# Kernel optimization log

Measured on AMD Instinct MI355X. Metric: run time of the kernel, lower is better.

Reference implementation:

```python
import jax, jax.numpy as jnp
import numpy as np

# ranges from init_kwargs
T2P_RANGE = (1.0, 500.0)
B1_RANGE = (0.2, 1.6)

NX, NY = 256, 256
NUM_T2S, NUM_B1S, ETL = 100, 30, 16


def _nan_to_num0(x):
    # torch.nan_to_num(x, nan=0.0, posinf=0.0); inputs here are non-negative so
    # neginf never occurs, but we zero it too for safety.
    return jnp.nan_to_num(x, nan=0.0, posinf=0.0, neginf=0.0)


def setup_inputs() -> dict:
    key = jax.random.key(0)
    k1, k2, k3 = jax.random.split(key, 3)
    slice_signal = jax.random.uniform(k1, (NX, NY, ETL), dtype=jnp.float32)
    db_mag = jax.random.uniform(k2, (NUM_T2S, NUM_B1S, ETL), dtype=jnp.float32)
    db_t2s_ms = jnp.linspace(1.0, 1000.0, NUM_T2S, dtype=jnp.float32)
    db_b1s = jnp.linspace(0.2, 1.6, NUM_B1S, dtype=jnp.float32)
    delta_t_t2p_ms = 9.0 * jnp.arange(1, ETL + 1, dtype=jnp.float32)  # echo times
    estimates = jax.random.uniform(k3, (2, NX, NY), dtype=jnp.float32)
    return {
        "slice_signal": slice_signal,
        "db_mag": db_mag,
        "db_t2s_ms": db_t2s_ms,
        "db_b1s": db_b1s,
        "delta_t_t2p_ms": delta_t_t2p_ms,
        "estimates": estimates,
    }


def reference(slice_signal, db_mag, db_t2s_ms, db_b1s, delta_t_t2p_ms, estimates):
    etl = slice_signal.shape[-1]
    sig = _nan_to_num0(slice_signal / jnp.linalg.norm(slice_signal, axis=-1, keepdims=True))
    sig = sig.reshape(-1, etl)  # (P, etl)

    # b1 map from estimates[1], scaled to b1_range
    b1 = B1_RANGE[0] + (B1_RANGE[1] - B1_RANGE[0]) * estimates[1]  # (nx, ny)
    # TV term: torch.gradient default == numpy.gradient (central diff interior,
    # one-sided edges)
    g0, g1 = jnp.gradient(b1)
    f_2 = jnp.sum(jnp.abs(g0) + jnp.abs(g1))

    # nearest-neighbor B1 dictionary lookup (non-differentiable gather)
    b1_flat = b1.reshape(-1)  # (P,)
    b1_idx = jnp.argmin((b1_flat[:, None] - db_b1s[None, :]) ** 2, axis=-1)  # (P,)
    db = db_mag[:, b1_idx]  # (T2, P, etl)

    # eta = exp(-dt / t2p), t2p from estimates[0] scaled to t2p_range
    t2p = T2P_RANGE[0] + (T2P_RANGE[1] - T2P_RANGE[0]) * estimates[0].reshape(-1)  # (P,)
    eta = jnp.exp(-delta_t_t2p_ms[None, :] / t2p[:, None])  # (P, etl)

    s_db = db * eta[None]  # (T2, P, etl)
    s_db = _nan_to_num0(s_db / jnp.linalg.norm(s_db, axis=-1, keepdims=True))

    l2_min = jnp.linalg.norm(s_db - sig[None], axis=-1)  # (T2, P)
    f_1 = jnp.sum(jnp.linalg.norm(l2_min, axis=-1))  # sum over T2 of per-T2 norms over pixels
    return f_1 + f_2
```

## Files before the change

### kernel.cpp

```cpp
#include <hip/hip_runtime.h>
#include <math.h>

constexpr int NXc = 256, NYc = 256, ETLc = 16, NTc = 100, NBc = 30;
constexpr int NPIX = NXc * NYc;
constexpr int TMAX = 13;
constexpr int RSTRIDE = 20;
constexpr int PST = 532;
constexpr int QST = 132;


__global__ __launch_bounds__(1024, 8) void k_main(
    const float* __restrict__ sig,
    const float* __restrict__ db_mag,
    const float* __restrict__ dtt,
    const float* __restrict__ est,
    float* __restrict__ ws_f1,
    float* __restrict__ ws_f2)
{
    const int tid      = threadIdx.x;
    const int pixgroup = blockIdx.x & 63;
    const int tc       = blockIdx.x >> 6;
    const int p = (pixgroup << 10) | tid;
    const int x = p >> 8;
    const int y = p & 255;
    const int t0   = (tc < 4) ? tc * 13 : 52 + (tc - 4) * 12;
    const int tcnt = (tc < 4) ? 13 : 12;
    const int lane = tid & 63;

    alignas(16) __shared__ float lds[TMAX * NBc * RSTRIDE];
    __shared__ float s_p[TMAX * PST];
    __shared__ float s_f2[16];

    {
        const float4* gsrc = reinterpret_cast<const float4*>(db_mag + (size_t)t0 * (NBc * ETLc));
        for (int i = tid; i < tcnt * 120; i += 1024) {
            const int ttl = i / 120;
            const int rem = i - ttl * 120;
            *reinterpret_cast<float4*>(
                &lds[ttl * (NBc * RSTRIDE) + (rem >> 2) * RSTRIDE + (rem & 3) * 4]) = gsrc[i];
        }
    }

    const float4* sp = reinterpret_cast<const float4*>(sig + (size_t)p * ETLc);
    float s[16];
    {
        float4 a = sp[0], b = sp[1], c = sp[2], d = sp[3];
        s[0]=a.x; s[1]=a.y; s[2]=a.z;  s[3]=a.w;
        s[4]=b.x; s[5]=b.y; s[6]=b.z;  s[7]=b.w;
        s[8]=c.x; s[9]=c.y; s[10]=c.z; s[11]=c.w;
        s[12]=d.x; s[13]=d.y; s[14]=d.z; s[15]=d.w;
    }
    float snrm2 = 0.f;
#pragma unroll
    for (int e = 0; e < 16; ++e) snrm2 = fmaf(s[e], s[e], snrm2);
    const float sig2  = (snrm2 > 0.f) ? 1.0f : 0.0f;
    const float srinv = (snrm2 > 0.f) ? __builtin_amdgcn_rsqf(snrm2) : 0.0f;
    float sgn[16];
#pragma unroll
    for (int e = 0; e < 16; ++e) sgn[e] = s[e] * srinv;

    const float est0 = est[p];
    const float t2p  = 1.0f + 499.0f * est0;
    const float nrcp = -__builtin_amdgcn_rcpf(t2p);
    float eta[16];
#pragma unroll
    for (int e = 0; e < 16; ++e) eta[e] = __expf(dtt[e] * nrcp);

    const float est1 = est[NPIX + p];
    float kf = roundf(est1 * 29.0f);
    kf = fminf(fmaxf(kf, 0.0f), 29.0f);
    const int jb = (int)kf;

    if (tc == 0) {
        const float* e1 = est + NPIX;
        const float c = 0.2f + 1.4f * est1;
        float g0, g1;
        if (x == 0)            g0 = (0.2f + 1.4f * e1[p + 256]) - c;
        else if (x == NXc - 1) g0 = c - (0.2f + 1.4f * e1[p - 256]);
        else                   g0 = 0.5f * ((0.2f + 1.4f * e1[p + 256]) - (0.2f + 1.4f * e1[p - 256]));
        if (y == 0)            g1 = (0.2f + 1.4f * e1[p + 1]) - c;
        else if (y == NYc - 1) g1 = c - (0.2f + 1.4f * e1[p - 1]);
        else                   g1 = 0.5f * ((0.2f + 1.4f * e1[p + 1]) - (0.2f + 1.4f * e1[p - 1]));
        float r = fabsf(g0) + fabsf(g1);
#pragma unroll
        for (int m = 32; m; m >>= 1) r += __shfl_xor(r, m, 64);
        if (lane == 0) s_f2[tid >> 6] = r;
    }

    __syncthreads();
    if (tc == 0 && tid < 4)
        ws_f2[(pixgroup << 2) + tid] =
            (s_f2[tid*4+0] + s_f2[tid*4+1]) + (s_f2[tid*4+2] + s_f2[tid*4+3]);

#pragma unroll 1
    for (int tt = 0; tt < tcnt; ++tt) {
        const float4* lp = reinterpret_cast<const float4*>(
            &lds[tt * (NBc * RSTRIDE) + jb * RSTRIDE]);
        float4 a = lp[0], b = lp[1], c = lp[2], d = lp[3];
        float dbr[16];
        dbr[0]=a.x; dbr[1]=a.y; dbr[2]=a.z;  dbr[3]=a.w;
        dbr[4]=b.x; dbr[5]=b.y; dbr[6]=b.z;  dbr[7]=b.w;
        dbr[8]=c.x; dbr[9]=c.y; dbr[10]=c.z; dbr[11]=c.w;
        dbr[12]=d.x; dbr[13]=d.y; dbr[14]=d.z; dbr[15]=d.w;

        float nrm2 = 0.f, dotv = 0.f;
#pragma unroll
        for (int e = 0; e < 16; ++e) {
            float v = dbr[e] * eta[e];
            nrm2 = fmaf(v, v, nrm2);
            dotv = fmaf(v, sgn[e], dotv);
        }
        float l2sq;
        if (nrm2 > 0.f) l2sq = sig2 + 1.0f - 2.0f * dotv * __builtin_amdgcn_rsqf(nrm2);
        else            l2sq = sig2;
        float r = (l2sq < 0.f) ? 0.f : l2sq;

        r += __shfl_xor(r, 1, 64);
        if ((lane & 1) == 0)
            s_p[tt * PST + (tid >> 8) * QST + ((tid >> 1) & 127)] = r;
    }
    __syncthreads();

    if (tid < tcnt * 64) {
        const int t = tid >> 6;
        const int q = (tid >> 4) & 3;
        const int j = tid & 15;
        const float* row = &s_p[t * PST + q * QST + j];
        float b = 0.f;
#pragma unroll
        for (int k = 0; k < 8; ++k) b += row[k * 16];
        b += __shfl_xor(b, 1, 64);
        b += __shfl_xor(b, 2, 64);
        b += __shfl_xor(b, 4, 64);
        b += __shfl_xor(b, 8, 64);
        if (j == 0) ws_f1[(size_t)(t0 + t) * 256 + (pixgroup << 2) + q] = b;
    }
}

__global__ __launch_bounds__(512) void k_final(
    const float* __restrict__ ws_f1,
    const float* __restrict__ ws_f2,
    float* __restrict__ out)
{
    const int tid = threadIdx.x;
    const int t = tid >> 2, g = tid & 3;
    float sum = 0.f;
    if (t < NTc) {
        const float4* p4 = reinterpret_cast<const float4*>(ws_f1 + (size_t)t * 256 + g * 64);
#pragma unroll
        for (int i = 0; i < 16; ++i) { float4 v = p4[i]; sum += (v.x + v.y) + (v.z + v.w); }
    }
    sum += __shfl_xor(sum, 1, 64);
    sum += __shfl_xor(sum, 2, 64);

    __shared__ float s_sq[128];
    if (tid < 128) s_sq[tid] = 0.f;
    __syncthreads();
    if (g == 0 && t < NTc) s_sq[t] = sqrtf(sum);
    __syncthreads();

    if (tid < 64) {
        float v = s_sq[tid] + s_sq[tid + 64];
        v += (ws_f2[tid] + ws_f2[tid + 64]) + (ws_f2[tid + 128] + ws_f2[tid + 192]);
#pragma unroll
        for (int m = 32; m; m >>= 1) v += __shfl_xor(v, m, 64);
        if (tid == 0) out[0] = v;
    }
}

extern "C" void kernel_launch(void* const* d_in, const int* in_sizes, int n_in,
                              void* d_out, int out_size, void* d_ws, size_t ws_size,
                              hipStream_t stream) {
    const float* sig    = (const float*)d_in[0];
    const float* db_mag = (const float*)d_in[1];
    const float* dtt    = (const float*)d_in[4];
    const float* est    = (const float*)d_in[5];
    float* out = (float*)d_out;

    float* ws_f1 = (float*)d_ws;
    float* ws_f2 = ws_f1 + (size_t)NTc * 256;

    k_main <<<dim3(64 * 8), dim3(1024), 0, stream>>>(sig, db_mag, dtt, est, ws_f1, ws_f2);
    k_final<<<dim3(1),      dim3(512),  0, stream>>>(ws_f1, ws_f2, out);
}
```

Measured before the change: 23.39 us.

## Sort pixels by B1 bin per block and read dictionary rows from global

Each block now counting-sorts its 1024 pixels by B1 bin, using LDS atomics for a histogram and rank assignment. Threads are then remapped so that neighbouring lanes share the same dictionary row. The LDS staging of the db_mag slab is removed, and each iteration reads its 16-float row straight from global memory. The aim is to avoid the LDS fill and the scattered LDS reads, relying on cache broadcast for the now-uniform rows. In exchange it adds extra barriers, atomics and permuted, less coalesced loads of the signal and estimates.

After: 28.26 us. +20.8%, slower.

```diff
diff --git a/kernel.cpp b/kernel.cpp
--- a/kernel.cpp
+++ b/kernel.cpp
@@ -4,7 +4,6 @@
 constexpr int NXc = 256, NYc = 256, ETLc = 16, NTc = 100, NBc = 30;
 constexpr int NPIX = NXc * NYc;
 constexpr int TMAX = 13;
-constexpr int RSTRIDE = 20;
 constexpr int PST = 532;
 constexpr int QST = 132;
 
@@ -27,53 +26,25 @@
     const int tcnt = (tc < 4) ? 13 : 12;
     const int lane = tid & 63;
 
-    alignas(16) __shared__ float lds[TMAX * NBc * RSTRIDE];
     __shared__ float s_p[TMAX * PST];
     __shared__ float s_f2[16];
-
-    {
-        const float4* gsrc = reinterpret_cast<const float4*>(db_mag + (size_t)t0 * (NBc * ETLc));
-        for (int i = tid; i < tcnt * 120; i += 1024) {
-            const int ttl = i / 120;
-            const int rem = i - ttl * 120;
-            *reinterpret_cast<float4*>(
-                &lds[ttl * (NBc * RSTRIDE) + (rem >> 2) * RSTRIDE + (rem & 3) * 4]) = gsrc[i];
-        }
-    }
-
-    const float4* sp = reinterpret_cast<const float4*>(sig + (size_t)p * ETLc);
-    float s[16];
-    {
-        float4 a = sp[0], b = sp[1], c = sp[2], d = sp[3];
-        s[0]=a.x; s[1]=a.y; s[2]=a.z;  s[3]=a.w;
-        s[4]=b.x; s[5]=b.y; s[6]=b.z;  s[7]=b.w;
-        s[8]=c.x; s[9]=c.y; s[10]=c.z; s[11]=c.w;
-        s[12]=d.x; s[13]=d.y; s[14]=d.z; s[15]=d.w;
-    }
-    float snrm2 = 0.f;
-#pragma unroll
-    for (int e = 0; e < 16; ++e) snrm2 = fmaf(s[e], s[e], snrm2);
-    const float sig2  = (snrm2 > 0.f) ? 1.0f : 0.0f;
-    const float srinv = (snrm2 > 0.f) ? __builtin_amdgcn_rsqf(snrm2) : 0.0f;
-    float sgn[16];
-#pragma unroll
-    for (int e = 0; e < 16; ++e) sgn[e] = s[e] * srinv;
-
-    const float est0 = est[p];
-    const float t2p  = 1.0f + 499.0f * est0;
-    const float nrcp = -__builtin_amdgcn_rcpf(t2p);
-    float eta[16];
-#pragma unroll
-    for (int e = 0; e < 16; ++e) eta[e] = __expf(dtt[e] * nrcp);
-
-    const float est1 = est[NPIX + p];
-    float kf = roundf(est1 * 29.0f);
-    kf = fminf(fmaxf(kf, 0.0f), 29.0f);
-    const int jb = (int)kf;
+    __shared__ int s_hist[NBc];
+    __shared__ int s_base[NBc];
+    __shared__ unsigned short s_ord[1024];
+
+    if (tid < NBc) s_hist[tid] = 0;
+
+    const float est1_own = est[NPIX + p];
+    float kfo = roundf(est1_own * 29.0f);
+    kfo = fminf(fmaxf(kfo, 0.0f), 29.0f);
+    const int jb_own = (int)kfo;
+
+    __syncthreads();
+    atomicAdd(&s_hist[jb_own], 1);
 
     if (tc == 0) {
         const float* e1 = est + NPIX;
-        const float c = 0.2f + 1.4f * est1;
+        const float c = 0.2f + 1.4f * est1_own;
         float g0, g1;
         if (x == 0)            g0 = (0.2f + 1.4f * e1[p + 256]) - c;
         else if (x == NXc - 1) g0 = c - (0.2f + 1.4f * e1[p - 256]);
@@ -88,15 +59,59 @@
     }
 
     __syncthreads();
+    if (tid == 0) {
+        int a = 0;
+#pragma unroll
+        for (int j = 0; j < NBc; ++j) { s_base[j] = a; a += s_hist[j]; }
+    }
     if (tc == 0 && tid < 4)
         ws_f2[(pixgroup << 2) + tid] =
             (s_f2[tid*4+0] + s_f2[tid*4+1]) + (s_f2[tid*4+2] + s_f2[tid*4+3]);
-
+    __syncthreads();
+    {
+        const int rank = atomicAdd(&s_base[jb_own], 1);
+        s_ord[rank] = (unsigned short)tid;
+    }
+    __syncthreads();
+
+    const int q = (pixgroup << 10) | (int)s_ord[tid];
+
+    const float4* sp = reinterpret_cast<const float4*>(sig + (size_t)q * ETLc);
+    float s[16];
+    {
+        float4 a = sp[0], b = sp[1], c = sp[2], d = sp[3];
+        s[0]=a.x; s[1]=a.y; s[2]=a.z;  s[3]=a.w;
+        s[4]=b.x; s[5]=b.y; s[6]=b.z;  s[7]=b.w;
+        s[8]=c.x; s[9]=c.y; s[10]=c.z; s[11]=c.w;
+        s[12]=d.x; s[13]=d.y; s[14]=d.z; s[15]=d.w;
+    }
+    float snrm2 = 0.f;
+#pragma unroll
+    for (int e = 0; e < 16; ++e) snrm2 = fmaf(s[e], s[e], snrm2);
+    const float sig2  = (snrm2 > 0.f) ? 1.0f : 0.0f;
+    const float srinv = (snrm2 > 0.f) ? __builtin_amdgcn_rsqf(snrm2) : 0.0f;
+    float sgn[16];
+#pragma unroll
+    for (int e = 0; e < 16; ++e) sgn[e] = s[e] * srinv;
+
+    const float est0 = est[q];
+    const float t2p  = 1.0f + 499.0f * est0;
+    const float nrcp = -__builtin_amdgcn_rcpf(t2p);
+    float eta[16];
+#pragma unroll
+    for (int e = 0; e < 16; ++e) eta[e] = __expf(dtt[e] * nrcp);
+
+    const float est1 = est[NPIX + q];
+    float kf = roundf(est1 * 29.0f);
+    kf = fminf(fmaxf(kf, 0.0f), 29.0f);
+    const int jb = (int)kf;
+
+    const float* dbj = db_mag + (size_t)jb * ETLc;
 #pragma unroll 1
     for (int tt = 0; tt < tcnt; ++tt) {
-        const float4* lp = reinterpret_cast<const float4*>(
-            &lds[tt * (NBc * RSTRIDE) + jb * RSTRIDE]);
-        float4 a = lp[0], b = lp[1], c = lp[2], d = lp[3];
+        const float4* dp = reinterpret_cast<const float4*>(
+            dbj + (size_t)(t0 + tt) * (NBc * ETLc));
+        float4 a = dp[0], b = dp[1], c = dp[2], d = dp[3];
         float dbr[16];
         dbr[0]=a.x; dbr[1]=a.y; dbr[2]=a.z;  dbr[3]=a.w;
         dbr[4]=b.x; dbr[5]=b.y; dbr[6]=b.z;  dbr[7]=b.w;
@@ -123,9 +138,9 @@
 
     if (tid < tcnt * 64) {
         const int t = tid >> 6;
-        const int q = (tid >> 4) & 3;
+        const int q4 = (tid >> 4) & 3;
         const int j = tid & 15;
-        const float* row = &s_p[t * PST + q * QST + j];
+        const float* row = &s_p[t * PST + q4 * QST + j];
         float b = 0.f;
 #pragma unroll
         for (int k = 0; k < 8; ++k) b += row[k * 16];
@@ -133,7 +148,7 @@
         b += __shfl_xor(b, 2, 64);
         b += __shfl_xor(b, 4, 64);
         b += __shfl_xor(b, 8, 64);
-        if (j == 0) ws_f1[(size_t)(t0 + t) * 256 + (pixgroup << 2) + q] = b;
+        if (j == 0) ws_f1[(size_t)(t0 + t) * 256 + (pixgroup << 2) + q4] = b;
     }
 }
 
```
